# Optimization experiments

Measured on AMD Instinct MI355X. Metric: run time of the kernel, lower is better.

Reference implementation:

```python
import jax, jax.numpy as jnp
import numpy as np

LEN_SORT_WINDOW = 2


def _butterfly_indices(v_len, d_v):
    # Column j is arange rolled right by s_j: s_0 = s_1 = 0, s_j = 2*(j-1) mod v_len.
    # (The butterfly_factor_to_matrix result in the original code is discarded;
    #  only the cyclic shifts matter.)
    shifts = np.zeros(d_v, dtype=np.int64)
    if d_v > 1:
        shifts[1:] = (LEN_SORT_WINDOW * np.arange(d_v - 1, dtype=np.int64)) % v_len
    rows = np.arange(v_len, dtype=np.int64)[:, None]
    return jnp.asarray((rows - shifts[None, :]) % v_len)  # [v_len, d_v] int64


def setup_inputs() -> dict:
    key = jax.random.key(0)
    B, L, D = 8, 4096, 1024
    v = jax.random.normal(key, (B, L, D), dtype=jnp.float32)
    return {"v": v}


def reference(v) -> jnp.ndarray:
    B, L, D = v.shape
    idx = _butterfly_indices(L, D)                       # [L, D]
    # gather: v_shifted[b,i,j] = v[b, idx[i,j], j]
    v_shifted = jnp.take_along_axis(v, jnp.broadcast_to(idx[None], (B, L, D)), axis=1)
    # windowed pairwise sort (ascending, window = 2) along the sequence dim
    pairs = v_shifted.reshape(B, L // LEN_SORT_WINDOW, LEN_SORT_WINDOW, D)
    v_sorted = jnp.sort(pairs, axis=2)
    return v_sorted.reshape(B, L, D)
```

## Files before the change

### kernel.cpp

```cpp
#include <hip/hip_runtime.h>

namespace {

constexpr int B  = 8;
constexpr int L  = 4096;
constexpr int D  = 1024;
constexpr int D4 = D / 4;
constexpr int P  = L / 2;
constexpr int TJ = 64;
constexpr int TP = 32;
constexpr int RP = TP + TJ;
constexpr int RR = 2 * RP;
constexpr int NT = 512;
constexpr int NW = NT / 64;
constexpr int NCH = RR * TJ * 4 / 1024;
constexpr int CPW = NCH / NW;
static_assert(CPW == 6, "chunk math");
static_assert(RR * TJ * 4 == 48 * 1024, "LDS = 48 KiB, 3 blocks/CU");

typedef float floatx4 __attribute__((ext_vector_type(4)));

__device__ __forceinline__ void async_ld16(const float* g, float* l) {
  __builtin_amdgcn_global_load_lds(
      (const __attribute__((address_space(1))) void*)g,
      (__attribute__((address_space(3))) void*)l, 16, 0, 0);
}

__global__ __launch_bounds__(NT, 6)
void swd_kernel(const float* __restrict__ v, float* __restrict__ out) {
  const int j0 = blockIdx.x * TJ;
  const int p0 = blockIdx.y * TP;
  const int b  = blockIdx.z;

  __shared__ float lds[RR * TJ];

  const int tid  = threadIdx.x;
  const int wave = tid >> 6;
  const int lane = tid & 63;

  const float* __restrict__ vb = v + (size_t)b * L * D + j0;
  const int r0 = p0 - (j0 + TJ - 2);

  const int f  = lane & 15;
  const int rc = lane >> 4;
#pragma unroll
  for (int i = 0; i < CPW; ++i) {
    const int C   = wave + NW * i;
    const int kr  = 4 * C + rc;
    const int q   = (r0 + (kr >> 1)) & (P - 1);
    const int row = 2 * q + (kr & 1);
    async_ld16(vb + (size_t)row * D + 4 * f, &lds[C * 256]);
  }
  asm volatile("s_waitcnt vmcnt(0)" ::: "memory");
  __syncthreads();

  const int g = tid & 15;
  const int c = tid >> 4;
  const int krb = 2 * c - 8 * g + 2 * (TJ - 1) - 6;
  const bool sp = (j0 == 0) && (g == 0);

  float4 m[4], M[4];
#pragma unroll
  for (int u = 0; u < 4; ++u) {
    const float4 a0 = *(const float4*)&lds[(krb + 2 * u)     * TJ + 4 * g];
    const float4 a1 = *(const float4*)&lds[(krb + 2 * u + 1) * TJ + 4 * g];
    m[u].x = fminf(a0.x, a1.x); M[u].x = fmaxf(a0.x, a1.x);
    m[u].y = fminf(a0.y, a1.y); M[u].y = fmaxf(a0.y, a1.y);
    m[u].z = fminf(a0.z, a1.z); M[u].z = fmaxf(a0.z, a1.z);
    m[u].w = fminf(a0.w, a1.w); M[u].w = fmaxf(a0.w, a1.w);
  }

  floatx4 e, o;
  e.x = sp ? m[2].x : m[3].x; e.y = m[2].y; e.z = m[1].z; e.w = m[0].w;
  o.x = sp ? M[2].x : M[3].x; o.y = M[2].y; o.z = M[1].z; o.w = M[0].w;

  float* __restrict__ ob = out + (size_t)b * L * D + j0 + 4 * g;
  const size_t ro = (size_t)(2 * (p0 + c)) * D;
  __builtin_nontemporal_store(e, (floatx4*)(ob + ro));
  __builtin_nontemporal_store(o, (floatx4*)(ob + ro + D));
}

}

extern "C" void kernel_launch(void* const* d_in, const int* , int ,
                              void* d_out, int , void* , size_t ,
                              hipStream_t stream) {
  const float* v = (const float*)d_in[0];
  float* out = (float*)d_out;
  dim3 grid(D / TJ, P / TP, B);
  swd_kernel<<<grid, NT, 0, stream>>>(v, out);
}
```

Before: 234.2 us.

## Process four column tiles per block and stage output through LDS

Each block now loops over four adjacent 64-column tiles, reusing the LDS buffer serially, and keeps the results in registers. The results are then staged through LDS so that each wave writes full 1 KiB contiguous row segments with nontemporal stores. The grid is flattened with batch as the fastest index to change the scheduling order. In exchange, loads and compute are serialized inside each block with no overlap between tiles, the block count drops by four, and extra barriers are added.

```diff
diff --git a/kernel.cpp b/kernel.cpp
--- a/kernel.cpp
+++ b/kernel.cpp
@@ -5,7 +5,6 @@
 constexpr int B  = 8;
 constexpr int L  = 4096;
 constexpr int D  = 1024;
-constexpr int D4 = D / 4;
 constexpr int P  = L / 2;
 constexpr int TJ = 64;
 constexpr int TP = 32;
@@ -13,10 +12,12 @@
 constexpr int RR = 2 * RP;
 constexpr int NT = 512;
 constexpr int NW = NT / 64;
+constexpr int GC = 4;
+constexpr int NXG = D / (GC * TJ);
 constexpr int NCH = RR * TJ * 4 / 1024;
 constexpr int CPW = NCH / NW;
 static_assert(CPW == 6, "chunk math");
-static_assert(RR * TJ * 4 == 48 * 1024, "LDS = 48 KiB, 3 blocks/CU");
+static_assert(RR * TJ * 4 == 48 * 1024, "LDS = 48 KiB");
 
 typedef float floatx4 __attribute__((ext_vector_type(4)));
 
@@ -28,9 +29,12 @@
 
 __global__ __launch_bounds__(NT, 6)
 void swd_kernel(const float* __restrict__ v, float* __restrict__ out) {
-  const int j0 = blockIdx.x * TJ;
-  const int p0 = blockIdx.y * TP;
-  const int b  = blockIdx.z;
+  const int bid  = blockIdx.x;
+  const int b    = bid & 7;
+  const int s    = bid >> 3;
+  const int x4   = s & 3;
+  const int band = s >> 2;
+  const int p0   = band * TP;
 
   __shared__ float lds[RR * TJ];
 
@@ -38,46 +42,74 @@
   const int wave = tid >> 6;
   const int lane = tid & 63;
 
-  const float* __restrict__ vb = v + (size_t)b * L * D + j0;
-  const int r0 = p0 - (j0 + TJ - 2);
-
   const int f  = lane & 15;
   const int rc = lane >> 4;
-#pragma unroll
-  for (int i = 0; i < CPW; ++i) {
-    const int C   = wave + NW * i;
-    const int kr  = 4 * C + rc;
-    const int q   = (r0 + (kr >> 1)) & (P - 1);
-    const int row = 2 * q + (kr & 1);
-    async_ld16(vb + (size_t)row * D + 4 * f, &lds[C * 256]);
-  }
-  asm volatile("s_waitcnt vmcnt(0)" ::: "memory");
-  __syncthreads();
 
   const int g = tid & 15;
   const int c = tid >> 4;
   const int krb = 2 * c - 8 * g + 2 * (TJ - 1) - 6;
-  const bool sp = (j0 == 0) && (g == 0);
 
-  float4 m[4], M[4];
+  const float* __restrict__ vb   = v   + (size_t)b * L * D;
+  float*       __restrict__ outb = out + (size_t)b * L * D;
+
+  float4 eG[GC], oG[GC];
+
 #pragma unroll
-  for (int u = 0; u < 4; ++u) {
-    const float4 a0 = *(const float4*)&lds[(krb + 2 * u)     * TJ + 4 * g];
-    const float4 a1 = *(const float4*)&lds[(krb + 2 * u + 1) * TJ + 4 * g];
-    m[u].x = fminf(a0.x, a1.x); M[u].x = fmaxf(a0.x, a1.x);
-    m[u].y = fminf(a0.y, a1.y); M[u].y = fmaxf(a0.y, a1.y);
-    m[u].z = fminf(a0.z, a1.z); M[u].z = fmaxf(a0.z, a1.z);
-    m[u].w = fminf(a0.w, a1.w); M[u].w = fmaxf(a0.w, a1.w);
+  for (int xx = 0; xx < GC; ++xx) {
+    const int x  = x4 * GC + xx;
+    const int j0 = x * TJ;
+    const int r0 = p0 - (j0 + TJ - 2);
+
+#pragma unroll
+    for (int i = 0; i < CPW; ++i) {
+      const int C   = wave + NW * i;
+      const int kr  = 4 * C + rc;
+      const int q   = (r0 + (kr >> 1)) & (P - 1);
+      const int row = 2 * q + (kr & 1);
+      async_ld16(vb + (size_t)row * D + j0 + 4 * f, &lds[C * 256]);
+    }
+    asm volatile("s_waitcnt vmcnt(0)" ::: "memory");
+    __syncthreads();
+
+    float4 m[4], M[4];
+#pragma unroll
+    for (int u = 0; u < 4; ++u) {
+      const float4 a0 = *(const float4*)&lds[(krb + 2 * u)     * TJ + 4 * g];
+      const float4 a1 = *(const float4*)&lds[(krb + 2 * u + 1) * TJ + 4 * g];
+      m[u].x = fminf(a0.x, a1.x); M[u].x = fmaxf(a0.x, a1.x);
+      m[u].y = fminf(a0.y, a1.y); M[u].y = fmaxf(a0.y, a1.y);
+      m[u].z = fminf(a0.z, a1.z); M[u].z = fmaxf(a0.z, a1.z);
+      m[u].w = fminf(a0.w, a1.w); M[u].w = fmaxf(a0.w, a1.w);
+    }
+    const bool sp = (j0 == 0) && (g == 0);
+    float4 e, o;
+    e.x = sp ? m[2].x : m[3].x; e.y = m[2].y; e.z = m[1].z; e.w = m[0].w;
+    o.x = sp ? M[2].x : M[3].x; o.y = M[2].y; o.z = M[1].z; o.w = M[0].w;
+    eG[xx] = e; oG[xx] = o;
+    __syncthreads();
   }
 
-  floatx4 e, o;
-  e.x = sp ? m[2].x : m[3].x; e.y = m[2].y; e.z = m[1].z; e.w = m[0].w;
-  o.x = sp ? M[2].x : M[3].x; o.y = M[2].y; o.z = M[1].z; o.w = M[0].w;
-
-  float* __restrict__ ob = out + (size_t)b * L * D + j0 + 4 * g;
-  const size_t ro = (size_t)(2 * (p0 + c)) * D;
-  __builtin_nontemporal_store(e, (floatx4*)(ob + ro));
-  __builtin_nontemporal_store(o, (floatx4*)(ob + ro + D));
+#pragma unroll
+  for (int h = 0; h < 2; ++h) {
+    if ((c >> 4) == h) {
+      const int r = 2 * c - 32 * h;
+#pragma unroll
+      for (int xx = 0; xx < GC; ++xx) {
+        *(float4*)&lds[(r    ) * 256 + 64 * xx + 4 * g] = eG[xx];
+        *(float4*)&lds[(r + 1) * 256 + 64 * xx + 4 * g] = oG[xx];
+      }
+    }
+    __syncthreads();
+#pragma unroll
+    for (int k = 0; k < 4; ++k) {
+      const int rl = 4 * wave + k;
+      const floatx4 val = *(const floatx4*)&lds[rl * 256 + 4 * lane];
+      __builtin_nontemporal_store(val,
+          (floatx4*)(outb + (size_t)(2 * p0 + 32 * h + rl) * D
+                     + 256 * x4 + 4 * lane));
+    }
+    __syncthreads();
+  }
 }
 
 }
@@ -87,6 +119,6 @@
                               hipStream_t stream) {
   const float* v = (const float*)d_in[0];
   float* out = (float*)d_out;
-  dim3 grid(D / TJ, P / TP, B);
+  dim3 grid(B * (P / TP) * NXG);
   swd_kernel<<<grid, NT, 0, stream>>>(v, out);
 }
```

Result: no change. 236.4 us (+0.9%).
